# Kernel optimization log

Measured on AMD Instinct MI355X. Metric: run time of the kernel, lower is better.

The kernel has to match this reference:

```python
import jax, jax.numpy as jnp
import numpy as np

N_NODES = 100000
N_EDGES = 1600000
F_IN = 64
F_HID = 64
CURV = 1.0          # fixed curvature for every layer (args.c)
MIN_NORM = 1e-15    # HGCN min_norm clamp
PROJ_EPS = 4e-3     # HGCN float32 boundary eps


def _artanh(x):
    x = jnp.clip(x, -1.0 + 1e-7, 1.0 - 1e-7)
    return 0.5 * (jnp.log1p(x) - jnp.log1p(-x))


def _norm(x):
    return jnp.sqrt(jnp.clip(jnp.sum(x * x, axis=-1, keepdims=True), MIN_NORM))


def proj(x, c):
    # clip points to the open Poincare ball of radius (1-eps)/sqrt(c)
    maxnorm = (1.0 - PROJ_EPS) / jnp.sqrt(c)
    n = _norm(x)
    return jnp.where(n > maxnorm, x / n * maxnorm, x)


def expmap0(u, c):
    sc = jnp.sqrt(c)
    n = _norm(u)
    return jnp.tanh(sc * n) * u / (sc * n)


def logmap0(p, c):
    sc = jnp.sqrt(c)
    n = _norm(p)
    return _artanh(sc * n) * p / (sc * n)


def mobius_add(x, y, c):
    x2 = jnp.sum(x * x, -1, keepdims=True)
    y2 = jnp.sum(y * y, -1, keepdims=True)
    xy = jnp.sum(x * y, -1, keepdims=True)
    num = (1.0 + 2.0 * c * xy + c * y2) * x + (1.0 - c * x2) * y
    den = 1.0 + 2.0 * c * xy + c * c * x2 * y2
    return num / jnp.clip(den, MIN_NORM)


def mobius_matvec(M, x, c):
    sc = jnp.sqrt(c)
    xn = _norm(x)
    mx = x @ M.T                       # [N, out]
    mxn = _norm(mx)
    res = jnp.tanh(mxn / xn * _artanh(sc * xn)) * mx / (mxn * sc)
    zero = jnp.all(mx == 0, axis=-1, keepdims=True)
    return jnp.where(zero, jnp.zeros_like(res), res)


def hyp_linear(x, W, b, c):
    res = proj(mobius_matvec(W, x, c), c)
    hyp_b = proj(expmap0(b.reshape(1, -1), c), c)   # proj_tan0 is identity on Poincare ball
    return proj(mobius_add(res, hyp_b, c), c)


def hyp_agg(x, src, dst, w, c, n_nodes):
    xt = logmap0(x, c)                              # tangent space at origin
    msg = xt[src] * w[:, None]                      # [E, d] gather + weight
    agg = jax.ops.segment_sum(msg, dst, num_segments=n_nodes)  # spmm(adj, xt)
    return proj(expmap0(agg, c), c)


def hyp_act(x, c_in, c_out):
    xt = jax.nn.relu(logmap0(x, c_in))              # act in tangent space
    return proj(expmap0(xt, c_out), c_out)          # proj_tan0 identity


def hgnn_layer(x, W, b, src, dst, w, c_in, c_out, n_nodes):
    h = hyp_linear(x, W, b, c_in)
    h = hyp_agg(h, src, dst, w, c_in, n_nodes)
    return hyp_act(h, c_in, c_out)


def setup_inputs() -> dict:
    key = jax.random.key(0)
    ks = jax.random.split(key, 7)
    x = jax.random.normal(ks[0], (N_NODES, F_IN), dtype=jnp.float32)
    edge_index = jax.random.randint(ks[1], (2, N_EDGES), 0, N_NODES, dtype=jnp.int64 if jax.config.jax_enable_x64 else jnp.int32)
    edge_weight = jax.random.uniform(ks[2], (N_EDGES,), dtype=jnp.float32) / 16.0
    W0 = jax.random.normal(ks[3], (F_HID, F_IN), dtype=jnp.float32) * 0.1
    b0 = jax.random.normal(ks[4], (F_HID,), dtype=jnp.float32) * 0.1
    W1 = jax.random.normal(ks[5], (F_HID, F_HID), dtype=jnp.float32) * 0.1
    b1 = jax.random.normal(ks[6], (F_HID,), dtype=jnp.float32) * 0.1
    return {"x": x, "edge_index": edge_index, "edge_weight": edge_weight,
            "W0": W0, "b0": b0, "W1": W1, "b1": b1}


def reference(x, edge_index, edge_weight, W0, b0, W1, b1):
    src, dst = edge_index[0], edge_index[1]
    # encode(): proj_tan0 (identity for Poincare ball) -> expmap0 -> proj
    h = proj(expmap0(x, CURV), CURV)
    h = hgnn_layer(h, W0, b0, src, dst, edge_weight, CURV, CURV, N_NODES)
    h = hgnn_layer(h, W1, b1, src, dst, edge_weight, CURV, CURV, N_NODES)
    return h
```

## Files before the change

kernel.cpp:

```cpp
#include <hip/hip_runtime.h>
#include <hip/hip_bf16.h>
#include <stdint.h>

#define MIN_NORM 1e-15f
#define MAXNORM 0.996f
#define ART_CLIP 0.9999999f
#define CAP 5120
#define BKT_NODES 256
#define W_SCALE 524288.f
#define W_INV   (1.f / 524288.f)

typedef __attribute__((ext_vector_type(8))) short s8v;
typedef __attribute__((ext_vector_type(4))) float f4v;

__device__ __forceinline__ float rcp_f(float x) { return __builtin_amdgcn_rcpf(x); }

__device__ __forceinline__ float fast_tanh(float x) {
    float e = __expf(2.f * x);
    return 1.f - 2.f * rcp_f(e + 1.f);
}
__device__ __forceinline__ float fast_artanh(float x) {
    x = fminf(x, ART_CLIP);
    return 0.5f * __logf((1.f + x) * rcp_f(1.f - x));
}

__device__ __forceinline__ float wsum(float v) {
#pragma unroll
    for (int m = 32; m >= 1; m >>= 1) v += __shfl_xor(v, m, 64);
    return v;
}
__device__ __forceinline__ unsigned wave_iscan(unsigned v, int lane) {
#pragma unroll
    for (int d = 1; d < 64; d <<= 1) {
        unsigned o = __shfl_up(v, d, 64);
        if (lane >= d) v += o;
    }
    return v;
}

__device__ __forceinline__ unsigned short f2bf(float f) {
    unsigned u = __builtin_bit_cast(unsigned, f);
    u += 0x7FFFu + ((u >> 16) & 1u);
    return (unsigned short)(u >> 16);
}
__device__ __forceinline__ float bf2f(unsigned short h) {
    return __builtin_bit_cast(float, (unsigned)h << 16);
}
__device__ __forceinline__ float bfu_lo(unsigned v) {
    return __builtin_bit_cast(float, v << 16);
}
__device__ __forceinline__ float bfu_hi(unsigned v) {
    return __builtin_bit_cast(float, v & 0xFFFF0000u);
}

__device__ __forceinline__ void part_body(const int* __restrict__ dst,
                                          const int* __restrict__ src,
                                          const float* __restrict__ ew,
                                          unsigned* __restrict__ bktCur,
                                          int2* __restrict__ part, int E, int NB,
                                          int blk, int PB) {
    __shared__ unsigned lcnt[512], lbase[512];
    const int tid = threadIdx.x;
    const int chunk = (E + PB - 1) / PB;
    const int lo = blk * chunk, hi = min(lo + chunk, E);
    for (int i = tid; i < NB; i += 256) lcnt[i] = 0;
    __syncthreads();
    for (int e = lo + tid; e < hi; e += 256)
        atomicAdd(&lcnt[(unsigned)dst[e] >> 8], 1u);
    __syncthreads();
    for (int i = tid; i < NB; i += 256) {
        unsigned c = lcnt[i];
        lbase[i] = c ? atomicAdd(&bktCur[i], c) : 0u;
        lcnt[i] = 0;
    }
    __syncthreads();
    for (int e = lo + tid; e < hi; e += 256) {
        int d = dst[e];
        int bkt = (unsigned)d >> 8;
        unsigned r = atomicAdd(&lcnt[bkt], 1u);
        unsigned rel = lbase[bkt] + r;
        if (rel < CAP)
            part[(size_t)bkt * CAP + rel] =
                make_int2(((d & 255) << 17) | src[e], __float_as_int(ew[e]));
    }
}

__global__ void __launch_bounds__(256) k_sort(const int2* __restrict__ part,
                                              const unsigned* __restrict__ bktCur,
                                              unsigned* __restrict__ part2,
                                              int2* __restrict__ off2, int nNodes) {
    const int b = blockIdx.x;
    const int base = b * CAP;
    const int cnt = min((int)bktCur[b], CAP);
    const int tid = threadIdx.x, lane = tid & 63, wid = tid >> 6;
    __shared__ unsigned hist[256];
    __shared__ unsigned wpart[4];
    hist[tid] = 0;
    __syncthreads();
    for (int i = tid; i < cnt; i += 256)
        atomicAdd(&hist[(unsigned)part[base + i].x >> 17], 1u);
    __syncthreads();
    unsigned h = hist[tid];
    unsigned inc = wave_iscan(h, lane);
    if (lane == 63) wpart[wid] = inc;
    __syncthreads();
    unsigned wo = 0;
    for (int i = 0; i < wid; ++i) wo += wpart[i];
    unsigned start = wo + inc - h;
    int node = b * BKT_NODES + tid;
    if (node < nNodes)
        off2[node] = make_int2(base + (int)start, base + (int)(start + h));
    __syncthreads();
    hist[tid] = start;
    __syncthreads();
    for (int i = tid; i < cnt; i += 256) {
        int2 m = part[base + i];
        unsigned r = atomicAdd(&hist[(unsigned)m.x >> 17], 1u);
        float w = __int_as_float(m.y);
        unsigned fw = (unsigned)__float2uint_rn(w * W_SCALE);
        if (fw > 32767u) fw = 32767u;
        part2[base + r] = (fw << 17) | ((unsigned)m.x & 0x1FFFFu);
    }
}

template <bool ENCODE>
__device__ __forceinline__ void lin_scalars(float n2, float m2, float d, float y2,
                                            float& lam, float& mu) {
    float nx = sqrtf(fmaxf(n2, MIN_NORM));
    float xn = ENCODE ? fminf(fast_tanh(nx), MAXNORM) : nx;
    float sm = sqrtf(fmaxf(m2, MIN_NORM));
    float ratio = sm * rcp_f(nx);
    float tt = fminf(fast_tanh(ratio * fast_artanh(xn)), MAXNORM);
    float rho = tt * rcp_f(sm);
    float xy = rho * d;
    float x2 = tt * tt;
    float den = fmaxf(1.f + 2.f * xy + x2 * y2, MIN_NORM);
    float iden = rcp_f(den);
    float A = (1.f + 2.f * xy + y2) * iden;
    float B = (1.f - x2) * iden;
    float on2 = A * A * x2 + 2.f * A * B * xy + B * B * y2;
    float on = sqrtf(fmaxf(on2, MIN_NORM));
    float g = on > MAXNORM ? MAXNORM * rcp_f(on) : 1.f;
    float onc = fminf(on, MAXNORM);
    float L = fast_artanh(onc) * rcp_f(onc) * g;
    lam = L * A * rho;
    mu  = L * B;
}

template <bool ENCODE>
__device__ __forceinline__ void lin_body(const float* __restrict__ xin,
                                         const float* __restrict__ W,
                                         const float* __restrict__ braw,
                                         unsigned short* __restrict__ xt_out,
                                         int nNodes, int nTiles, int blk, int LB) {
    __shared__ float shb[65];
    const int tid = threadIdx.x;
    if (tid < 64) {
        float u = braw[tid];
        float n = sqrtf(fmaxf(wsum(u * u), MIN_NORM));
        float t = tanhf(n);
        float h = t * u / n;
        float hn = sqrtf(fmaxf(wsum(h * h), MIN_NORM));
        if (hn > MAXNORM) h *= MAXNORM / hn;
        shb[tid] = h;
        float y2 = wsum(h * h);
        if (tid == 0) shb[64] = y2;
    }
    __syncthreads();

    const int lane = tid & 63, wid = tid >> 6;
    const int col = lane & 15, q = lane >> 4;

    s8v wfh[4][2], wfl[4][2];
    float hbr[4][4];
#pragma unroll
    for (int f = 0; f < 4; ++f) {
#pragma unroll
        for (int s = 0; s < 2; ++s) {
            const float4 a4 = *(const float4*)(W + (size_t)(16 * f + col) * 64 + 4 * q + 32 * s);
            const float4 b4 = *(const float4*)(W + (size_t)(16 * f + col) * 64 + 4 * q + 16 + 32 * s);
            float v[8] = {a4.x, a4.y, a4.z, a4.w, b4.x, b4.y, b4.z, b4.w};
            s8v h8, l8;
#pragma unroll
            for (int e = 0; e < 8; ++e) {
                unsigned short hb_ = f2bf(v[e]);
                float hf = bf2f(hb_);
                h8[e] = (short)hb_;
                l8[e] = (short)f2bf(v[e] - hf);
            }
            wfh[f][s] = h8;
            wfl[f][s] = l8;
        }
#pragma unroll
        for (int r = 0; r < 4; ++r) hbr[f][r] = shb[16 * f + 4 * q + r];
    }
    const float y2 = shb[64];

    const int nw = LB * 4;
    for (int t = blk * 4 + wid; t < nTiles; t += nw) {
        const int node = t * 16 + col;
        const bool ok = node < nNodes;
        const int ldn = ok ? node : (nNodes - 1);
        float n2p = 0.f;
        s8v xh[2], xl[2];
#pragma unroll
        for (int s = 0; s < 2; ++s) {
            const float4 a4 = *(const float4*)(xin + (size_t)ldn * 64 + 4 * q + 32 * s);
            const float4 b4 = *(const float4*)(xin + (size_t)ldn * 64 + 4 * q + 16 + 32 * s);
            float xv[8] = {a4.x, a4.y, a4.z, a4.w, b4.x, b4.y, b4.z, b4.w};
            s8v h8, l8;
#pragma unroll
            for (int e = 0; e < 8; ++e) {
                float xe = xv[e];
                n2p = fmaf(xe, xe, n2p);
                unsigned short hb_ = f2bf(xe);
                float hf = bf2f(hb_);
                h8[e] = (short)hb_;
                l8[e] = (short)f2bf(xe - hf);
            }
            xh[s] = h8;
            xl[s] = l8;
        }
        f4v acc[4];
#pragma unroll
        for (int f = 0; f < 4; ++f) acc[f] = (f4v){0.f, 0.f, 0.f, 0.f};
#pragma unroll
        for (int s = 0; s < 2; ++s) {
#pragma unroll
            for (int f = 0; f < 4; ++f)
                acc[f] = __builtin_amdgcn_mfma_f32_16x16x32_bf16(wfh[f][s], xh[s], acc[f], 0, 0, 0);
#pragma unroll
            for (int f = 0; f < 4; ++f)
                acc[f] = __builtin_amdgcn_mfma_f32_16x16x32_bf16(wfh[f][s], xl[s], acc[f], 0, 0, 0);
#pragma unroll
            for (int f = 0; f < 4; ++f)
                acc[f] = __builtin_amdgcn_mfma_f32_16x16x32_bf16(wfl[f][s], xh[s], acc[f], 0, 0, 0);
        }
        float m2p = 0.f, dp = 0.f;
#pragma unroll
        for (int f = 0; f < 4; ++f)
#pragma unroll
            for (int r = 0; r < 4; ++r) {
                float mv = acc[f][r];
                m2p = fmaf(mv, mv, m2p);
                dp  = fmaf(mv, hbr[f][r], dp);
            }
#pragma unroll
        for (int m = 16; m <= 32; m <<= 1) {
            n2p += __shfl_xor(n2p, m, 64);
            m2p += __shfl_xor(m2p, m, 64);
            dp  += __shfl_xor(dp,  m, 64);
        }
        float lam, mu;
        lin_scalars<ENCODE>(n2p, m2p, dp, y2, lam, mu);
        if (ok) {
#pragma unroll
            for (int f = 0; f < 4; ++f) {
                float r0 = fmaf(lam, acc[f][0], mu * hbr[f][0]);
                float r1 = fmaf(lam, acc[f][1], mu * hbr[f][1]);
                float r2 = fmaf(lam, acc[f][2], mu * hbr[f][2]);
                float r3 = fmaf(lam, acc[f][3], mu * hbr[f][3]);
                uint2 pk;
                pk.x = (unsigned)f2bf(r0) | ((unsigned)f2bf(r1) << 16);
                pk.y = (unsigned)f2bf(r2) | ((unsigned)f2bf(r3) << 16);
                *(uint2*)(xt_out + (size_t)node * 64 + 16 * f + 4 * q) = pk;
            }
        }
    }
}

__global__ void __launch_bounds__(256, 2) k_pre(const int* __restrict__ dst,
                                                const int* __restrict__ src,
                                                const float* __restrict__ ew,
                                                unsigned* __restrict__ bktCur,
                                                int2* __restrict__ part, int E, int NB,
                                                const float* __restrict__ x,
                                                const float* __restrict__ W0,
                                                const float* __restrict__ b0,
                                                unsigned short* __restrict__ xt,
                                                int nNodes, int nTiles, int PB, int LB) {
    if ((int)blockIdx.x < PB)
        part_body(dst, src, ew, bktCur, part, E, NB, blockIdx.x, PB);
    else
        lin_body<true>(x, W0, b0, xt, nNodes, nTiles, blockIdx.x - PB, LB);
}

template <bool ENCODE>
__global__ void __launch_bounds__(256, 2) k_lin(const float* __restrict__ xin,
                                                const float* __restrict__ W,
                                                const float* __restrict__ braw,
                                                unsigned short* __restrict__ xt_out,
                                                int nNodes, int nTiles) {
    lin_body<ENCODE>(xin, W, braw, xt_out, nNodes, nTiles, blockIdx.x, gridDim.x);
}

__global__ void __launch_bounds__(256) k_agg(const unsigned short* __restrict__ xt,
                                             const unsigned* __restrict__ meta,
                                             const int2* __restrict__ off2,
                                             float* __restrict__ hout, int nNodes) {
    const int tid = threadIdx.x;
    const int lane = tid & 63;
    const int h = lane >> 5;
    const int j = lane & 31;
    const int hbase = h << 5;
    const int nw = gridDim.x * (blockDim.x >> 6);
    const int nPairs = (nNodes + 1) >> 1;
    int pair = blockIdx.x * (blockDim.x >> 6) + (tid >> 6);
    if (pair >= nPairs) return;
    int node = pair * 2 + h;
    int2 rng = (node < nNodes) ? off2[node] : make_int2(0, 0);
    while (true) {
        const int nxt = pair + nw;
        int2 rngN = make_int2(0, 0);
        if (nxt < nPairs) {
            int nn = nxt * 2 + h;
            if (nn < nNodes) rngN = off2[nn];
        }
        const bool okn = node < nNodes;
        const int s0 = rng.x;
        const int deg = rng.y - rng.x;
        unsigned mp = 0;
        if (j < deg) mp = meta[s0 + j];
        const int kmax = min(deg, 32);
        const int kOther = __shfl(kmax, lane ^ 32, 64);
        const int kCeil = (max(kmax, kOther) + 7) & ~7;
        float a0 = 0.f, a1 = 0.f, b0_ = 0.f, b1_ = 0.f;
        for (int k = 0; k < kCeil; k += 8) {
            unsigned p0 = __shfl(mp, hbase + k, 64);
            unsigned p1 = __shfl(mp, hbase + k + 1, 64);
            unsigned p2 = __shfl(mp, hbase + k + 2, 64);
            unsigned p3 = __shfl(mp, hbase + k + 3, 64);
            unsigned p4 = __shfl(mp, hbase + k + 4, 64);
            unsigned p5 = __shfl(mp, hbase + k + 5, 64);
            unsigned p6 = __shfl(mp, hbase + k + 6, 64);
            unsigned p7 = __shfl(mp, hbase + k + 7, 64);
            unsigned v0 = *(const unsigned*)(xt + (((p0 & 0x1FFFFu) << 6) + 2 * j));
            unsigned v1 = *(const unsigned*)(xt + (((p1 & 0x1FFFFu) << 6) + 2 * j));
            unsigned v2 = *(const unsigned*)(xt + (((p2 & 0x1FFFFu) << 6) + 2 * j));
            unsigned v3 = *(const unsigned*)(xt + (((p3 & 0x1FFFFu) << 6) + 2 * j));
            unsigned v4 = *(const unsigned*)(xt + (((p4 & 0x1FFFFu) << 6) + 2 * j));
            unsigned v5 = *(const unsigned*)(xt + (((p5 & 0x1FFFFu) << 6) + 2 * j));
            unsigned v6 = *(const unsigned*)(xt + (((p6 & 0x1FFFFu) << 6) + 2 * j));
            unsigned v7 = *(const unsigned*)(xt + (((p7 & 0x1FFFFu) << 6) + 2 * j));
            float w0 = (float)(p0 >> 17);
            float w1 = (float)(p1 >> 17);
            float w2 = (float)(p2 >> 17);
            float w3 = (float)(p3 >> 17);
            float w4 = (float)(p4 >> 17);
            float w5 = (float)(p5 >> 17);
            float w6 = (float)(p6 >> 17);
            float w7 = (float)(p7 >> 17);
            a0 = fmaf(bfu_lo(v0), w0, a0);   a1 = fmaf(bfu_hi(v0), w0, a1);
            b0_ = fmaf(bfu_lo(v1), w1, b0_); b1_ = fmaf(bfu_hi(v1), w1, b1_);
            a0 = fmaf(bfu_lo(v2), w2, a0);   a1 = fmaf(bfu_hi(v2), w2, a1);
            b0_ = fmaf(bfu_lo(v3), w3, b0_); b1_ = fmaf(bfu_hi(v3), w3, b1_);
            a0 = fmaf(bfu_lo(v4), w4, a0);   a1 = fmaf(bfu_hi(v4), w4, a1);
            b0_ = fmaf(bfu_lo(v5), w5, b0_); b1_ = fmaf(bfu_hi(v5), w5, b1_);
            a0 = fmaf(bfu_lo(v6), w6, a0);   a1 = fmaf(bfu_hi(v6), w6, a1);
            b0_ = fmaf(bfu_lo(v7), w7, b0_); b1_ = fmaf(bfu_hi(v7), w7, b1_);
        }
        for (int kk = s0 + 32; kk < rng.y; ++kk) {
            unsigned pv = meta[kk];
            unsigned v = *(const unsigned*)(xt + (((pv & 0x1FFFFu) << 6) + 2 * j));
            float wv2 = (float)(pv >> 17);
            a0 = fmaf(bfu_lo(v), wv2, a0);
            a1 = fmaf(bfu_hi(v), wv2, a1);
        }
        float acc0 = (a0 + b0_) * W_INV, acc1 = (a1 + b1_) * W_INV;
        float r0 = fmaxf(acc0, 0.f), r1 = fmaxf(acc1, 0.f);
        float sA = fmaf(acc0, acc0, acc1 * acc1);
        float sR = fmaf(r0, r0, r1 * r1);
#pragma unroll
        for (int mm = 1; mm <= 16; mm <<= 1) {
            sA += __shfl_xor(sA, mm, 64);
            sR += __shfl_xor(sR, mm, 64);
        }
        float n = sqrtf(fmaxf(sA, MIN_NORM));
        float t = fast_tanh(n);
        float g1 = t > MAXNORM ? MAXNORM * rcp_f(t) : 1.f;
        float tc = fminf(t, MAXNORM);
        float alpha = fast_artanh(tc) * rcp_f(tc) * g1 * t * rcp_f(n);
        float mnorm = sqrtf(fmaxf(alpha * alpha * sR, MIN_NORM));
        float t2 = fast_tanh(mnorm);
        float g2 = t2 > MAXNORM ? MAXNORM * rcp_f(t2) : 1.f;
        float gamma = t2 * rcp_f(mnorm) * g2 * alpha;
        if (okn) {
            float2 o;
            o.x = gamma * r0;
            o.y = gamma * r1;
            *(float2*)(hout + (size_t)node * 64 + 2 * j) = o;
        }
        if (nxt >= nPairs) break;
        pair = nxt;
        node = pair * 2 + h;
        rng = rngN;
    }
}

extern "C" void kernel_launch(void* const* d_in, const int* in_sizes, int n_in,
                              void* d_out, int out_size, void* d_ws, size_t ws_size,
                              hipStream_t stream) {
    const float* x   = (const float*)d_in[0];
    const int*   ei  = (const int*)d_in[1];
    const float* ew  = (const float*)d_in[2];
    const float* W0  = (const float*)d_in[3];
    const float* b0  = (const float*)d_in[4];
    const float* W1  = (const float*)d_in[5];
    const float* b1  = (const float*)d_in[6];
    const int N = in_sizes[0] / 64;
    const int E = in_sizes[2];
    const int* src = ei;
    const int* dst = ei + E;
    const int NB = (N + BKT_NODES - 1) / BKT_NODES;
    const int nTiles = (N + 15) / 16;
    const int PB = 512, LB = 1536;

    uint8_t* p = (uint8_t*)d_ws;
    auto carve = [&](size_t bytes) { uint8_t* q = p; p += (bytes + 255) & ~(size_t)255; return q; };
    unsigned*       bktCur = (unsigned*)carve((size_t)NB * 4);
    int2*           part   = (int2*)carve((size_t)NB * CAP * 8);
    unsigned*       part2  = (unsigned*)carve((size_t)NB * CAP * 4);
    int2*           off2   = (int2*)carve((size_t)N * 8);
    unsigned short* xt     = (unsigned short*)carve((size_t)N * 64 * 2);
    float*          hbuf   = (float*)d_out;

    hipMemsetAsync(bktCur, 0, (size_t)NB * 4, stream);
    k_pre<<<PB + LB, 256, 0, stream>>>(dst, src, ew, bktCur, part, E, NB,
                                       x, W0, b0, xt, N, nTiles, PB, LB);
    k_sort<<<NB, 256, 0, stream>>>(part, bktCur, part2, off2, N);

    k_agg<<<2048, 256, 0, stream>>>(xt, part2, off2, hbuf, N);
    k_lin<false><<<1024, 256, 0, stream>>>(hbuf, W1, b1, xt, N, nTiles);
    k_agg<<<2048, 256, 0, stream>>>(xt, part2, off2, (float*)d_out, N);
}
```

Before: 165.7 us.

## Co-schedule encode linear with bucket sort instead of with partitioning

The first-layer encode/linear work moves out of the edge-partition kernel and into the bucket-sort kernel, so partitioning now runs alone in a 256-block kernel. The sort blocks and the linear tiles share one launch, letting the dense work fill idle CUs while the sort runs. The partition grid shrinks from 512 to 256 blocks and the linear block count from 1536 to 1024, which changes per-block edge chunk sizes and atomic contention.

Measured after the change: 161.9 us. 2.3% less time.

```diff
diff --git a/kernel.cpp b/kernel.cpp
--- a/kernel.cpp
+++ b/kernel.cpp
@@ -53,16 +53,16 @@
     return __builtin_bit_cast(float, v & 0xFFFF0000u);
 }
 
-__device__ __forceinline__ void part_body(const int* __restrict__ dst,
-                                          const int* __restrict__ src,
-                                          const float* __restrict__ ew,
-                                          unsigned* __restrict__ bktCur,
-                                          int2* __restrict__ part, int E, int NB,
-                                          int blk, int PB) {
+__global__ void __launch_bounds__(256) k_part(const int* __restrict__ dst,
+                                              const int* __restrict__ src,
+                                              const float* __restrict__ ew,
+                                              unsigned* __restrict__ bktCur,
+                                              int2* __restrict__ part, int E, int NB) {
     __shared__ unsigned lcnt[512], lbase[512];
     const int tid = threadIdx.x;
+    const int PB = gridDim.x;
     const int chunk = (E + PB - 1) / PB;
-    const int lo = blk * chunk, hi = min(lo + chunk, E);
+    const int lo = blockIdx.x * chunk, hi = min(lo + chunk, E);
     for (int i = tid; i < NB; i += 256) lcnt[i] = 0;
     __syncthreads();
     for (int e = lo + tid; e < hi; e += 256)
@@ -85,11 +85,10 @@
     }
 }
 
-__global__ void __launch_bounds__(256) k_sort(const int2* __restrict__ part,
-                                              const unsigned* __restrict__ bktCur,
-                                              unsigned* __restrict__ part2,
-                                              int2* __restrict__ off2, int nNodes) {
-    const int b = blockIdx.x;
+__device__ __forceinline__ void sort_body(const int2* __restrict__ part,
+                                          const unsigned* __restrict__ bktCur,
+                                          unsigned* __restrict__ part2,
+                                          int2* __restrict__ off2, int nNodes, int b) {
     const int base = b * CAP;
     const int cnt = min((int)bktCur[b], CAP);
     const int tid = threadIdx.x, lane = tid & 63, wid = tid >> 6;
@@ -269,20 +268,19 @@
     }
 }
 
-__global__ void __launch_bounds__(256, 2) k_pre(const int* __restrict__ dst,
-                                                const int* __restrict__ src,
-                                                const float* __restrict__ ew,
-                                                unsigned* __restrict__ bktCur,
-                                                int2* __restrict__ part, int E, int NB,
+__global__ void __launch_bounds__(256, 2) k_mid(const int2* __restrict__ part,
+                                                const unsigned* __restrict__ bktCur,
+                                                unsigned* __restrict__ part2,
+                                                int2* __restrict__ off2, int NB,
                                                 const float* __restrict__ x,
                                                 const float* __restrict__ W0,
                                                 const float* __restrict__ b0,
                                                 unsigned short* __restrict__ xt,
-                                                int nNodes, int nTiles, int PB, int LB) {
-    if ((int)blockIdx.x < PB)
-        part_body(dst, src, ew, bktCur, part, E, NB, blockIdx.x, PB);
+                                                int nNodes, int nTiles, int LB) {
+    if ((int)blockIdx.x < NB)
+        sort_body(part, bktCur, part2, off2, nNodes, blockIdx.x);
     else
-        lin_body<true>(x, W0, b0, xt, nNodes, nTiles, blockIdx.x - PB, LB);
+        lin_body<true>(x, W0, b0, xt, nNodes, nTiles, blockIdx.x - NB, LB);
 }
 
 template <bool ENCODE>
@@ -413,7 +411,7 @@
     const int* dst = ei + E;
     const int NB = (N + BKT_NODES - 1) / BKT_NODES;
     const int nTiles = (N + 15) / 16;
-    const int PB = 512, LB = 1536;
+    const int LB = 1024;
 
     uint8_t* p = (uint8_t*)d_ws;
     auto carve = [&](size_t bytes) { uint8_t* q = p; p += (bytes + 255) & ~(size_t)255; return q; };
@@ -425,10 +423,9 @@
     float*          hbuf   = (float*)d_out;
 
     hipMemsetAsync(bktCur, 0, (size_t)NB * 4, stream);
-    k_pre<<<PB + LB, 256, 0, stream>>>(dst, src, ew, bktCur, part, E, NB,
-                                       x, W0, b0, xt, N, nTiles, PB, LB);
-    k_sort<<<NB, 256, 0, stream>>>(part, bktCur, part2, off2, N);
-
+    k_part<<<256, 256, 0, stream>>>(dst, src, ew, bktCur, part, E, NB);
+    k_mid<<<NB + LB, 256, 0, stream>>>(part, bktCur, part2, off2, NB,
+                                       x, W0, b0, xt, N, nTiles, LB);
     k_agg<<<2048, 256, 0, stream>>>(xt, part2, off2, hbuf, N);
     k_lin<false><<<1024, 256, 0, stream>>>(hbuf, W1, b1, xt, N, nTiles);
     k_agg<<<2048, 256, 0, stream>>>(xt, part2, off2, (float*)d_out, N);
```
